# Optimization experiments

Hardware: AMD Instinct MI355X
Metric: run time of the kernel (lower is better)

The kernel has to match this reference:

```python
import jax, jax.numpy as jnp
import numpy as np

N = 100000   # nodes
E = 1600000  # edges
IN = 128
HID = 128
OUT = 64
H = 4
DH = HID // H  # 32
EPS = 1e-5


def gatconv(x, W, al, ar, b, src, dst, heads, dh, act):
    """DGL GATConv: fc -> edge attn (leaky_relu 0.2) -> segment softmax over dst -> scatter sum -> bias -> act."""
    feat = (x @ W).reshape(-1, heads, dh)            # [N,H,dh]
    el = (feat * al).sum(-1)                          # [N,H]
    er = (feat * ar).sum(-1)                          # [N,H]
    e = jax.nn.leaky_relu(el[src] + er[dst], 0.2)     # [E,H]
    m = jax.ops.segment_max(e, dst, num_segments=N)   # [N,H]
    ex = jnp.exp(e - m[dst])                          # [E,H]
    s = jax.ops.segment_sum(ex, dst, num_segments=N)  # [N,H]
    alpha = ex / s[dst]                               # [E,H]
    msg = alpha[:, :, None] * feat[src]               # [E,H,dh]
    out = jax.ops.segment_sum(msg, dst, num_segments=N)  # [N,H,dh]
    out = out + b.reshape(1, heads, dh)
    return act(out) if act is not None else out


def layernorm(x, g, beta):
    mu = x.mean(-1, keepdims=True)
    var = ((x - mu) ** 2).mean(-1, keepdims=True)
    return (x - mu) * jax.lax.rsqrt(var + EPS) * g + beta


def setup_inputs():
    key = jax.random.key(0)
    ks = jax.random.split(key, 24)
    rn = lambda k, shape, s=0.05: jax.random.normal(k, shape, dtype=jnp.float32) * s
    return {
        "x": jax.random.normal(ks[0], (N, IN), dtype=jnp.float32),
        "src": jax.random.randint(ks[1], (E,), 0, N, dtype=jnp.int32),
        "dst": jax.random.randint(ks[2], (E,), 0, N, dtype=jnp.int32),
        "W0": rn(ks[3], (IN, H * DH)), "al0": rn(ks[4], (H, DH)), "ar0": rn(ks[5], (H, DH)), "b0": jnp.zeros((H * DH,), jnp.float32),
        "W1": rn(ks[6], (HID, H * DH)), "al1": rn(ks[7], (H, DH)), "ar1": rn(ks[8], (H, DH)), "b1": jnp.zeros((H * DH,), jnp.float32),
        "W2": rn(ks[9], (HID, HID)), "al2": rn(ks[10], (1, HID)), "ar2": rn(ks[11], (1, HID)), "b2": jnp.zeros((HID,), jnp.float32),
        "g0": jnp.ones((HID,), jnp.float32), "be0": jnp.zeros((HID,), jnp.float32),
        "g1": jnp.ones((HID,), jnp.float32), "be1": jnp.zeros((HID,), jnp.float32),
        "Wc": rn(ks[12], (HID, OUT)), "bc": jnp.zeros((OUT,), jnp.float32),
    }


def reference(x, src, dst, W0, al0, ar0, b0, W1, al1, ar1, b1, W2, al2, ar2, b2,
              g0, be0, g1, be1, Wc, bc):
    # layer 0 (heads=4, elu) -> flatten -> residual -> LN (dropout in eval = identity)
    h_res = x
    h = gatconv(x, W0, al0, ar0, b0, src, dst, H, DH, jax.nn.elu).reshape(N, HID)
    h = layernorm(h + h_res, g0, be0)
    # layer 1 (heads=4, elu)
    h_res = h
    h = gatconv(h, W1, al1, ar1, b1, src, dst, H, DH, jax.nn.elu).reshape(N, HID)
    h = layernorm(h + h_res, g1, be1)
    # layer 2 (heads=1, no activation) -> squeeze -> residual, no norm
    h_res = h
    h = gatconv(h, W2, al2, ar2, b2, src, dst, 1, HID, None).reshape(N, HID)
    h = h + h_res
    embedding = h
    logits = embedding @ Wc + bc
    return (logits, embedding)
```

## Files before the change

### kernel.cpp

```cpp
#include <hip/hip_runtime.h>

#define NN 100000
#define EE 1600000
#define BSHIFT 9
#define NBKT ((NN + 511) / 512)
#define CAP 10240
#define CHUNK 2048
#define NBLKA ((EE + CHUNK - 1) / CHUNK)

typedef float f32x4 __attribute__((ext_vector_type(4)));
typedef float f32x2 __attribute__((ext_vector_type(2)));
typedef short s16x8 __attribute__((ext_vector_type(8)));

__device__ __forceinline__ ushort f2bf(float x) {
  uint u = __float_as_uint(x);
  return (ushort)((u + 0x7fffu + ((u >> 16) & 1u)) >> 16);
}
__device__ __forceinline__ uint pack2bf(float x, float y) {
  return (uint)f2bf(x) | ((uint)f2bf(y) << 16);
}
__device__ __forceinline__ float bflo(uint p) { return __uint_as_float(p << 16); }
__device__ __forceinline__ float bfhi(uint p) { return __uint_as_float(p & 0xffff0000u); }

template<int M, bool ABF, int ELER>
__global__ __launch_bounds__(256) void gemm_mfma(const void* __restrict__ Av,
    const float* __restrict__ W, const float* __restrict__ bias,
    float* __restrict__ outf, ushort* __restrict__ feat8s,
    const float* __restrict__ al, const float* __restrict__ ar,
    float* __restrict__ el, float* __restrict__ er, int N) {
  __shared__ ushort Wt[M * 136];
  const int tid = threadIdx.x;
  for (int idx = tid; idx < 128 * M; idx += 256) {
    int k = idx / M, c = idx - k * M;
    Wt[c * 136 + k] = f2bf(W[idx]);
  }
  __syncthreads();
  const int wid = tid >> 6, lane = tid & 63;
  const int rl = lane & 15, grp = lane >> 4;
  const long row0 = (long)blockIdx.x * 128;

  s16x8 af[2][4];
#pragma unroll
  for (int rt = 0; rt < 2; ++rt) {
    long row = row0 + rt * 64 + wid * 16 + rl;
    if (row >= N) row = N - 1;
    if (ABF) {
      const s16x8* Ar = (const s16x8*)((const ushort*)Av + row * 128);
#pragma unroll
      for (int ks = 0; ks < 4; ++ks) af[rt][ks] = Ar[ks * 4 + grp];
    } else {
      const float4* Ar = (const float4*)((const float*)Av + row * 128);
#pragma unroll
      for (int ks = 0; ks < 4; ++ks) {
        float4 a0 = Ar[ks * 8 + grp * 2];
        float4 a1 = Ar[ks * 8 + grp * 2 + 1];
        s16x8 f;
        f[0] = (short)f2bf(a0.x); f[1] = (short)f2bf(a0.y);
        f[2] = (short)f2bf(a0.z); f[3] = (short)f2bf(a0.w);
        f[4] = (short)f2bf(a1.x); f[5] = (short)f2bf(a1.y);
        f[6] = (short)f2bf(a1.z); f[7] = (short)f2bf(a1.w);
        af[rt][ks] = f;
      }
    }
  }
  const int NT = M / 16;
  f32x4 acc[2][NT];
#pragma unroll
  for (int rt = 0; rt < 2; ++rt)
#pragma unroll
    for (int ct = 0; ct < NT; ++ct) acc[rt][ct] = (f32x4)(0.f);

#pragma unroll
  for (int ct = 0; ct < NT; ++ct) {
#pragma unroll
    for (int ks = 0; ks < 4; ++ks) {
      s16x8 bf = *(const s16x8*)&Wt[(ct * 16 + rl) * 136 + ks * 32 + grp * 8];
      acc[0][ct] = __builtin_amdgcn_mfma_f32_16x16x32_bf16(af[0][ks], bf, acc[0][ct], 0, 0, 0);
      acc[1][ct] = __builtin_amdgcn_mfma_f32_16x16x32_bf16(af[1][ks], bf, acc[1][ct], 0, 0, 0);
    }
  }

  if (ELER > 0) __syncthreads();

#pragma unroll
  for (int rt = 0; rt < 2; ++rt) {
#pragma unroll
    for (int ct = 0; ct < NT; ++ct) {
      int col = ct * 16 + rl;
      float bb = (ELER == 0) ? bias[col] : 0.f;
#pragma unroll
      for (int j = 0; j < 4; ++j) {
        int lrow = rt * 64 + wid * 16 + grp * 4 + j;
        long grow = row0 + lrow;
        if (ELER > 0) {
          Wt[lrow * 128 + col] = f2bf(acc[rt][ct][j]);
        } else if (grow < N) {
          outf[grow * M + col] = acc[rt][ct][j] + bb;
        }
      }
    }
  }

  if (ELER > 0) {
    __syncthreads();
    const uint* stage = (const uint*)Wt;
    float2 a2 = ((const float2*)al)[lane];
    float2 r2 = ((const float2*)ar)[lane];
    for (int rr = 0; rr < 32; ++rr) {
      int lrow = wid * 32 + rr;
      long grow = row0 + lrow;
      uint p = stage[lrow * 64 + lane];
      float x0 = bflo(p), x1 = bfhi(p);
      int pk8 = __builtin_amdgcn_cvt_pk_fp8_f32(x0, x1, 0, false);
      if (grow < N) feat8s[grow * 64 + lane] = (ushort)pk8;
      float pl = x0 * a2.x + x1 * a2.y;
      float pr = x0 * r2.x + x1 * r2.y;
      if (ELER == 4) {
#pragma unroll
        for (int m = 8; m; m >>= 1) {
          pl += __shfl_xor(pl, m, 16);
          pr += __shfl_xor(pr, m, 16);
        }
        if ((lane & 15) == 0 && grow < N) {
          el[grow * 4 + (lane >> 4)] = pl;
          er[grow * 4 + (lane >> 4)] = pr;
        }
      } else {
#pragma unroll
        for (int m = 32; m; m >>= 1) {
          pl += __shfl_xor(pl, m, 64);
          pr += __shfl_xor(pr, m, 64);
        }
        if (lane == 0 && grow < N) { el[grow] = pl; er[grow] = pr; }
      }
    }
  }
}

template<int HEADS>
__global__ __launch_bounds__(256) void wcomp(const int* __restrict__ ssrc,
    const int* __restrict__ sdst, const float* __restrict__ el,
    const float* __restrict__ er, float* __restrict__ wcsr) {
  int e = blockIdx.x * 256 + threadIdx.x;
  if (e >= EE) return;
  int sn = ssrc[e], dn = sdst[e];
  if (HEADS == 4) {
    float4 l4 = ((const float4*)el)[sn];
    float4 r4 = ((const float4*)er)[dn];
    float4 w;
    float ev;
    ev = l4.x + r4.x; ev = fmaxf(ev, 0.f) + 0.2f * fminf(ev, 0.f); w.x = __expf(ev);
    ev = l4.y + r4.y; ev = fmaxf(ev, 0.f) + 0.2f * fminf(ev, 0.f); w.y = __expf(ev);
    ev = l4.z + r4.z; ev = fmaxf(ev, 0.f) + 0.2f * fminf(ev, 0.f); w.z = __expf(ev);
    ev = l4.w + r4.w; ev = fmaxf(ev, 0.f) + 0.2f * fminf(ev, 0.f); w.w = __expf(ev);
    ((float4*)wcsr)[e] = w;
  } else {
    float ev = el[sn] + er[dn];
    ev = fmaxf(ev, 0.f) + 0.2f * fminf(ev, 0.f);
    wcsr[e] = __expf(ev);
  }
}

__global__ __launch_bounds__(256) void k_partA(const int* __restrict__ src,
    const int* __restrict__ dst, uint* __restrict__ bcnt, uint* __restrict__ tmp) {
  __shared__ uint hist[NBKT], excl[NBKT], gbase[NBKT], cur[NBKT];
  __shared__ uint2 recs[CHUNK];
  const int t = threadIdx.x;
  const long e0 = (long)blockIdx.x * CHUNK;
  const int cnt = (EE - e0 < CHUNK) ? (int)(EE - e0) : CHUNK;
  for (int i = t; i < NBKT; i += 256) hist[i] = 0;
  __syncthreads();
  for (int i = t; i < cnt; i += 256) {
    int d = dst[e0 + i];
    atomicAdd(&hist[d >> BSHIFT], 1u);
  }
  __syncthreads();
  if (t == 0) {
    uint run = 0;
    for (int i = 0; i < NBKT; ++i) { excl[i] = run; run += hist[i]; }
  }
  __syncthreads();
  if (t < NBKT) {
    gbase[t] = atomicAdd(&bcnt[t], hist[t]);
    cur[t] = excl[t];
  }
  __syncthreads();
  for (int i = t; i < cnt; i += 256) {
    uint s = (uint)src[e0 + i], d = (uint)dst[e0 + i];
    uint p = atomicAdd(&cur[d >> BSHIFT], 1u);
    recs[p] = make_uint2(s, d);
  }
  __syncthreads();
  for (int i = t; i < cnt; i += 256) {
    uint2 r = recs[i];
    uint b = r.y >> BSHIFT;
    uint pos = gbase[b] + ((uint)i - excl[b]);
    if (pos < CAP) tmp[(long)b * CAP + pos] = r.x | ((r.y & 511u) << 17);
  }
}

__global__ __launch_bounds__(256) void k_bscan(const uint* __restrict__ bcnt,
    uint* __restrict__ bbase, int* __restrict__ indptr) {
  __shared__ uint lds[NBKT];
  int t = threadIdx.x;
  if (t < NBKT) lds[t] = bcnt[t];
  __syncthreads();
  if (t == 0) {
    uint run = 0;
    for (int i = 0; i < NBKT; ++i) { bbase[i] = run; run += lds[i]; }
    indptr[NN] = (int)run;
  }
}

__global__ __launch_bounds__(256) void k_partB(const uint* __restrict__ bcnt,
    const uint* __restrict__ bbase, const uint* __restrict__ tmp,
    int* __restrict__ indptr, int* __restrict__ ssrc, int* __restrict__ sdst) {
  __shared__ uint hist[512], cur[512], wsum[256];
  __shared__ uint stage[CAP];
  const int b = blockIdx.x, t = threadIdx.x;
  const int dlo = b << BSHIFT;
  const int nn = (NN - dlo < 512) ? (NN - dlo) : 512;
  int nrec = (int)bcnt[b];
  if (nrec > CAP) nrec = CAP;
  const uint base = bbase[b];
  const uint* tb = tmp + (long)b * CAP;
  for (int i = t; i < 512; i += 256) hist[i] = 0;
  __syncthreads();
  for (int i = t; i < nrec; i += 256) {
    atomicAdd(&hist[tb[i] >> 17], 1u);
  }
  __syncthreads();
  uint a0 = hist[t * 2], a1 = hist[t * 2 + 1];
  uint ts = a0 + a1;
  wsum[t] = ts;
  __syncthreads();
  for (int st = 1; st < 256; st <<= 1) {
    uint v = (t >= st) ? wsum[t - st] : 0;
    __syncthreads();
    wsum[t] += v;
    __syncthreads();
  }
  uint texcl = wsum[t] - ts;
  cur[t * 2] = texcl;
  cur[t * 2 + 1] = texcl + a0;
  if (t * 2 < nn)     indptr[dlo + t * 2]     = (int)(base + texcl);
  if (t * 2 + 1 < nn) indptr[dlo + t * 2 + 1] = (int)(base + texcl + a0);
  __syncthreads();
  for (int i = t; i < nrec; i += 256) {
    uint v = tb[i];
    uint rel = atomicAdd(&cur[v >> 17], 1u);
    stage[rel] = v;
  }
  __syncthreads();
  for (int i = t; i < nrec; i += 256) {
    uint v = stage[i];
    ssrc[base + i] = (int)(v & 0x1FFFFu);
    sdst[base + i] = dlo + (int)(v >> 17);
  }
}

template<int HEADS, bool FINAL, bool PREVBF>
__global__ __launch_bounds__(256) void gat_aggregate(
    const int* __restrict__ indptr, const int* __restrict__ ssrc,
    const float* __restrict__ wcsr, const char* __restrict__ feat8,
    const float* __restrict__ bias, const void* __restrict__ prevv,
    const float* __restrict__ g, const float* __restrict__ beta,
    void* __restrict__ outv, int N) {
  int wave = threadIdx.x >> 6, lane = threadIdx.x & 63;
  long n = (long)blockIdx.x * 4 + wave;
  if (n >= N) return;
  const int b = __builtin_amdgcn_readfirstlane(indptr[n]);
  const int e = __builtin_amdgcn_readfirstlane(indptr[n + 1]);
  const int deg = e - b;
  const int l5 = lane & 31, half = lane >> 5;
  const int* sp = ssrc + b;
  const float* wlp;
  if (HEADS == 4) wlp = wcsr + (size_t)b * 4 + half * 4 + (l5 >> 3);
  else            wlp = wcsr + (size_t)b + half;
  const uint lpart = (uint)l5 * 4u;

  float a0 = 0.f, a1 = 0.f, a2 = 0.f, a3 = 0.f, s = 0.f;
  const int npair = (deg + 1) >> 1;
  for (int p = 0; p < npair; p += 4) {
#pragma unroll
    for (int k = 0; k < 4; ++k) {
      const int pk = p + k;
      int ja = 2 * pk;     if (ja > deg - 1) ja = deg - 1;
      int jb = 2 * pk + 1; if (jb > deg - 1) jb = deg - 1;
      uint sao = ((uint)sp[ja] & 131071u) << 7;
      uint sbo = ((uint)sp[jb] & 131071u) << 7;
      uint voff = (half ? sbo : sao) + lpart;
      uint v = *(const uint*)(feat8 + voff);
      float w = (HEADS == 4) ? wlp[(size_t)k * 8] : wlp[(size_t)k * 2];
      w = (2 * pk + half < deg) ? w : 0.f;
      auto f01 = __builtin_amdgcn_cvt_pk_f32_fp8((int)v, false);
      auto f23 = __builtin_amdgcn_cvt_pk_f32_fp8((int)v, true);
      s += w;
      a0 = fmaf(w, f01[0], a0);
      a1 = fmaf(w, f01[1], a1);
      a2 = fmaf(w, f23[0], a2);
      a3 = fmaf(w, f23[1], a3);
    }
    wlp += (HEADS == 4) ? 32 : 8;
  }
  a0 += __shfl_xor(a0, 32, 64);
  a1 += __shfl_xor(a1, 32, 64);
  a2 += __shfl_xor(a2, 32, 64);
  a3 += __shfl_xor(a3, 32, 64);
  s  += __shfl_xor(s, 32, 64);

  float inv = (s > 0.f) ? 1.f / s : 0.f;
  float v0 = a0 * inv, v1 = a1 * inv, v2 = a2 * inv, v3 = a3 * inv;
  float4 bb = ((const float4*)bias)[l5];
  v0 += bb.x; v1 += bb.y; v2 += bb.z; v3 += bb.w;
  if (!FINAL) {
    v0 = v0 > 0.f ? v0 : __expf(v0) - 1.f;
    v1 = v1 > 0.f ? v1 : __expf(v1) - 1.f;
    v2 = v2 > 0.f ? v2 : __expf(v2) - 1.f;
    v3 = v3 > 0.f ? v3 : __expf(v3) - 1.f;
  }
  if (PREVBF) {
    uint2 pp = ((const uint2*)prevv)[n * 32 + l5];
    v0 += bflo(pp.x); v1 += bfhi(pp.x);
    v2 += bflo(pp.y); v3 += bfhi(pp.y);
  } else {
    float4 ph = ((const float4*)prevv)[n * 32 + l5];
    v0 += ph.x; v1 += ph.y; v2 += ph.z; v3 += ph.w;
  }
  if (!FINAL) {
    float sum = v0 + v1 + v2 + v3;
#pragma unroll
    for (int m = 16; m; m >>= 1) sum += __shfl_xor(sum, m, 64);
    float mu = sum * (1.f / 128.f);
    float d0 = v0 - mu, d1 = v1 - mu, d2 = v2 - mu, d3 = v3 - mu;
    float vs = d0 * d0 + d1 * d1 + d2 * d2 + d3 * d3;
#pragma unroll
    for (int m = 16; m; m >>= 1) vs += __shfl_xor(vs, m, 64);
    float rstd = rsqrtf(vs * (1.f / 128.f) + 1e-5f);
    float4 g4 = ((const float4*)g)[l5];
    float4 be4 = ((const float4*)beta)[l5];
    float o0 = d0 * rstd * g4.x + be4.x;
    float o1 = d1 * rstd * g4.y + be4.y;
    float o2 = d2 * rstd * g4.z + be4.z;
    float o3 = d3 * rstd * g4.w + be4.w;
    if (!half) ((uint2*)outv)[n * 32 + l5] = make_uint2(pack2bf(o0, o1), pack2bf(o2, o3));
  } else {
    if (!half) ((float4*)outv)[n * 32 + l5] = make_float4(v0, v1, v2, v3);
  }
}

extern "C" void kernel_launch(void* const* d_in, const int* in_sizes, int n_in,
                              void* d_out, int out_size, void* d_ws, size_t ws_size,
                              hipStream_t stream) {
  const float* x   = (const float*)d_in[0];
  const int*   src = (const int*)d_in[1];
  const int*   dst = (const int*)d_in[2];
  const float* W0  = (const float*)d_in[3];
  const float* al0 = (const float*)d_in[4];
  const float* ar0 = (const float*)d_in[5];
  const float* b0  = (const float*)d_in[6];
  const float* W1  = (const float*)d_in[7];
  const float* al1 = (const float*)d_in[8];
  const float* ar1 = (const float*)d_in[9];
  const float* b1  = (const float*)d_in[10];
  const float* W2  = (const float*)d_in[11];
  const float* al2 = (const float*)d_in[12];
  const float* ar2 = (const float*)d_in[13];
  const float* b2  = (const float*)d_in[14];
  const float* g0  = (const float*)d_in[15];
  const float* be0 = (const float*)d_in[16];
  const float* g1  = (const float*)d_in[17];
  const float* be1 = (const float*)d_in[18];
  const float* Wc  = (const float*)d_in[19];
  const float* bc  = (const float*)d_in[20];

  float* out    = (float*)d_out;
  float* logits = out;
  float* emb    = out + (long)NN * 64;

  char*   feat8 = (char*)d_ws;
  float*  el    = (float*)(feat8 + (size_t)NN * 128);
  float*  er    = el + (long)NN * 4;
  ushort* bufAb = (ushort*)(er + (long)NN * 4);
  ushort* bufBb = bufAb + (long)NN * 128;
  float*  wcsrb = (float*)(bufBb + (long)NN * 128);
  int*    sdst  = (int*)(wcsrb + (long)EE * 4);
  uint*   tmp   = (uint*)(sdst + EE);
  uint*   bcnt  = tmp + (long)NBKT * CAP;
  uint*   bbase = bcnt + NBKT;
  ushort* feat8s = (ushort*)feat8;

  int* indptr = (int*)d_out;
  int* ssrc   = indptr + NN + 1;

  const int gN4 = (NN + 3) / 4;
  const int gGm = (NN + 127) / 128;
  const int gE  = (EE + 255) / 256;

  hipMemsetAsync(bcnt, 0, NBKT * sizeof(uint), stream);
  k_partA<<<NBLKA, 256, 0, stream>>>(src, dst, bcnt, tmp);
  k_bscan<<<1, 256, 0, stream>>>(bcnt, bbase, indptr);
  k_partB<<<NBKT, 256, 0, stream>>>(bcnt, bbase, tmp, indptr, ssrc, sdst);

  gemm_mfma<128, false, 4><<<gGm, 256, 0, stream>>>(x, W0, nullptr, nullptr, feat8s, al0, ar0, el, er, NN);
  wcomp<4><<<gE, 256, 0, stream>>>(ssrc, sdst, el, er, wcsrb);
  gat_aggregate<4, false, false><<<gN4, 256, 0, stream>>>(indptr, ssrc, wcsrb, feat8, b0, x, g0, be0, bufAb, NN);

  gemm_mfma<128, true, 4><<<gGm, 256, 0, stream>>>(bufAb, W1, nullptr, nullptr, feat8s, al1, ar1, el, er, NN);
  wcomp<4><<<gE, 256, 0, stream>>>(ssrc, sdst, el, er, wcsrb);
  gat_aggregate<4, false, true><<<gN4, 256, 0, stream>>>(indptr, ssrc, wcsrb, feat8, b1, bufAb, g1, be1, bufBb, NN);

  gemm_mfma<128, true, 1><<<gGm, 256, 0, stream>>>(bufBb, W2, nullptr, nullptr, feat8s, al2, ar2, el, er, NN);
  wcomp<1><<<gE, 256, 0, stream>>>(ssrc, sdst, el, er, wcsrb);
  gat_aggregate<1, true, true><<<gN4, 256, 0, stream>>>(indptr, ssrc, wcsrb, feat8, b2, bufBb, nullptr, nullptr, emb, NN);

  gemm_mfma<64, false, 0><<<gGm, 256, 0, stream>>>(emb, Wc, bc, logits, nullptr, nullptr, nullptr, nullptr, nullptr, NN);
}
```

Before: 362.9 us.

## Process four edges per wave iteration with 8-byte fp8 gathers per lane

Restructures the per-node aggregation so each wave splits into four 16-lane groups, each handling one edge per iteration and loading 8 fp8 features per lane. The old layout used two 32-lane halves with 4 bytes per lane. Accumulation now uses packed f32x2 multiply-adds, and the ragged tail gets a single masked step. The goal is more gather parallelism and wider loads per instruction, at the cost of a two-stage cross-group shuffle reduction and more registers per lane. The old mask of source indices (&131071) is dropped.

```diff
diff --git a/kernel.cpp b/kernel.cpp
--- a/kernel.cpp
+++ b/kernel.cpp
@@ -272,80 +272,116 @@
   const int b = __builtin_amdgcn_readfirstlane(indptr[n]);
   const int e = __builtin_amdgcn_readfirstlane(indptr[n + 1]);
   const int deg = e - b;
-  const int l5 = lane & 31, half = lane >> 5;
+  const int l4 = lane & 15, q = lane >> 4;
+  const int head = (HEADS == 4) ? (l4 >> 2) : 0;
   const int* sp = ssrc + b;
-  const float* wlp;
-  if (HEADS == 4) wlp = wcsr + (size_t)b * 4 + half * 4 + (l5 >> 3);
-  else            wlp = wcsr + (size_t)b + half;
-  const uint lpart = (uint)l5 * 4u;
-
-  float a0 = 0.f, a1 = 0.f, a2 = 0.f, a3 = 0.f, s = 0.f;
-  const int npair = (deg + 1) >> 1;
-  for (int p = 0; p < npair; p += 4) {
-#pragma unroll
-    for (int k = 0; k < 4; ++k) {
-      const int pk = p + k;
-      int ja = 2 * pk;     if (ja > deg - 1) ja = deg - 1;
-      int jb = 2 * pk + 1; if (jb > deg - 1) jb = deg - 1;
-      uint sao = ((uint)sp[ja] & 131071u) << 7;
-      uint sbo = ((uint)sp[jb] & 131071u) << 7;
-      uint voff = (half ? sbo : sao) + lpart;
-      uint v = *(const uint*)(feat8 + voff);
-      float w = (HEADS == 4) ? wlp[(size_t)k * 8] : wlp[(size_t)k * 2];
-      w = (2 * pk + half < deg) ? w : 0.f;
-      auto f01 = __builtin_amdgcn_cvt_pk_f32_fp8((int)v, false);
-      auto f23 = __builtin_amdgcn_cvt_pk_f32_fp8((int)v, true);
-      s += w;
-      a0 = fmaf(w, f01[0], a0);
-      a1 = fmaf(w, f01[1], a1);
-      a2 = fmaf(w, f23[0], a2);
-      a3 = fmaf(w, f23[1], a3);
-    }
-    wlp += (HEADS == 4) ? 32 : 8;
-  }
-  a0 += __shfl_xor(a0, 32, 64);
-  a1 += __shfl_xor(a1, 32, 64);
-  a2 += __shfl_xor(a2, 32, 64);
-  a3 += __shfl_xor(a3, 32, 64);
-  s  += __shfl_xor(s, 32, 64);
+  const float* wl = wcsr + (size_t)b * HEADS + q * HEADS + head;
+  const uint lpart = (uint)l4 * 8u;
+
+  f32x2 ac0 = {0.f, 0.f}, ac1 = {0.f, 0.f}, ac2 = {0.f, 0.f}, ac3 = {0.f, 0.f};
+  float s = 0.f;
+  const int ngrp = deg >> 2;
+#pragma unroll 2
+  for (int kk = 0; kk < ngrp; ++kk) {
+    int sn0 = sp[4 * kk + 0], sn1 = sp[4 * kk + 1];
+    int sn2 = sp[4 * kk + 2], sn3 = sp[4 * kk + 3];
+    uint so0 = (uint)sn0 << 7, so1 = (uint)sn1 << 7;
+    uint so2 = (uint)sn2 << 7, so3 = (uint)sn3 << 7;
+    uint so = (q == 0) ? so0 : (q == 1) ? so1 : (q == 2) ? so2 : so3;
+    uint2 v = *(const uint2*)(feat8 + (so + lpart));
+    float w = wl[(size_t)kk * 4 * HEADS];
+    s += w;
+    f32x2 w2 = {w, w};
+    ac0 += w2 * __builtin_amdgcn_cvt_pk_f32_fp8((int)v.x, false);
+    ac1 += w2 * __builtin_amdgcn_cvt_pk_f32_fp8((int)v.x, true);
+    ac2 += w2 * __builtin_amdgcn_cvt_pk_f32_fp8((int)v.y, false);
+    ac3 += w2 * __builtin_amdgcn_cvt_pk_f32_fp8((int)v.y, true);
+  }
+  if (deg & 3) {
+    int j = 4 * ngrp + q;
+    int jc = j < deg - 1 ? j : deg - 1;
+    uint sn = (uint)ssrc[b + jc];
+    uint2 v = *(const uint2*)(feat8 + (((uint)sn << 7) + lpart));
+    float w = wcsr[(size_t)(b + jc) * HEADS + head];
+    w = (j < deg) ? w : 0.f;
+    s += w;
+    f32x2 w2 = {w, w};
+    ac0 += w2 * __builtin_amdgcn_cvt_pk_f32_fp8((int)v.x, false);
+    ac1 += w2 * __builtin_amdgcn_cvt_pk_f32_fp8((int)v.x, true);
+    ac2 += w2 * __builtin_amdgcn_cvt_pk_f32_fp8((int)v.y, false);
+    ac3 += w2 * __builtin_amdgcn_cvt_pk_f32_fp8((int)v.y, true);
+  }
+#pragma unroll
+  for (int m = 16; m <= 32; m <<= 1) {
+    ac0[0] += __shfl_xor(ac0[0], m, 64); ac0[1] += __shfl_xor(ac0[1], m, 64);
+    ac1[0] += __shfl_xor(ac1[0], m, 64); ac1[1] += __shfl_xor(ac1[1], m, 64);
+    ac2[0] += __shfl_xor(ac2[0], m, 64); ac2[1] += __shfl_xor(ac2[1], m, 64);
+    ac3[0] += __shfl_xor(ac3[0], m, 64); ac3[1] += __shfl_xor(ac3[1], m, 64);
+    s += __shfl_xor(s, m, 64);
+  }
 
   float inv = (s > 0.f) ? 1.f / s : 0.f;
-  float v0 = a0 * inv, v1 = a1 * inv, v2 = a2 * inv, v3 = a3 * inv;
-  float4 bb = ((const float4*)bias)[l5];
-  v0 += bb.x; v1 += bb.y; v2 += bb.z; v3 += bb.w;
+  float v0 = ac0[0] * inv, v1 = ac0[1] * inv, v2 = ac1[0] * inv, v3 = ac1[1] * inv;
+  float v4 = ac2[0] * inv, v5 = ac2[1] * inv, v6 = ac3[0] * inv, v7 = ac3[1] * inv;
+  float4 bl = ((const float4*)bias)[l4 * 2];
+  float4 bh = ((const float4*)bias)[l4 * 2 + 1];
+  v0 += bl.x; v1 += bl.y; v2 += bl.z; v3 += bl.w;
+  v4 += bh.x; v5 += bh.y; v6 += bh.z; v7 += bh.w;
   if (!FINAL) {
     v0 = v0 > 0.f ? v0 : __expf(v0) - 1.f;
     v1 = v1 > 0.f ? v1 : __expf(v1) - 1.f;
     v2 = v2 > 0.f ? v2 : __expf(v2) - 1.f;
     v3 = v3 > 0.f ? v3 : __expf(v3) - 1.f;
+    v4 = v4 > 0.f ? v4 : __expf(v4) - 1.f;
+    v5 = v5 > 0.f ? v5 : __expf(v5) - 1.f;
+    v6 = v6 > 0.f ? v6 : __expf(v6) - 1.f;
+    v7 = v7 > 0.f ? v7 : __expf(v7) - 1.f;
   }
   if (PREVBF) {
-    uint2 pp = ((const uint2*)prevv)[n * 32 + l5];
+    uint4 pp = ((const uint4*)prevv)[n * 16 + l4];
     v0 += bflo(pp.x); v1 += bfhi(pp.x);
     v2 += bflo(pp.y); v3 += bfhi(pp.y);
+    v4 += bflo(pp.z); v5 += bfhi(pp.z);
+    v6 += bflo(pp.w); v7 += bfhi(pp.w);
   } else {
-    float4 ph = ((const float4*)prevv)[n * 32 + l5];
-    v0 += ph.x; v1 += ph.y; v2 += ph.z; v3 += ph.w;
+    float4 pl = ((const float4*)prevv)[n * 32 + l4 * 2];
+    float4 ph = ((const float4*)prevv)[n * 32 + l4 * 2 + 1];
+    v0 += pl.x; v1 += pl.y; v2 += pl.z; v3 += pl.w;
+    v4 += ph.x; v5 += ph.y; v6 += ph.z; v7 += ph.w;
   }
   if (!FINAL) {
-    float sum = v0 + v1 + v2 + v3;
-#pragma unroll
-    for (int m = 16; m; m >>= 1) sum += __shfl_xor(sum, m, 64);
+    float sum = ((v0 + v1) + (v2 + v3)) + ((v4 + v5) + (v6 + v7));
+#pragma unroll
+    for (int m = 8; m; m >>= 1) sum += __shfl_xor(sum, m, 64);
     float mu = sum * (1.f / 128.f);
     float d0 = v0 - mu, d1 = v1 - mu, d2 = v2 - mu, d3 = v3 - mu;
-    float vs = d0 * d0 + d1 * d1 + d2 * d2 + d3 * d3;
-#pragma unroll
-    for (int m = 16; m; m >>= 1) vs += __shfl_xor(vs, m, 64);
+    float d4 = v4 - mu, d5 = v5 - mu, d6 = v6 - mu, d7 = v7 - mu;
+    float vs = ((d0 * d0 + d1 * d1) + (d2 * d2 + d3 * d3)) +
+               ((d4 * d4 + d5 * d5) + (d6 * d6 + d7 * d7));
+#pragma unroll
+    for (int m = 8; m; m >>= 1) vs += __shfl_xor(vs, m, 64);
     float rstd = rsqrtf(vs * (1.f / 128.f) + 1e-5f);
-    float4 g4 = ((const float4*)g)[l5];
-    float4 be4 = ((const float4*)beta)[l5];
-    float o0 = d0 * rstd * g4.x + be4.x;
-    float o1 = d1 * rstd * g4.y + be4.y;
-    float o2 = d2 * rstd * g4.z + be4.z;
-    float o3 = d3 * rstd * g4.w + be4.w;
-    if (!half) ((uint2*)outv)[n * 32 + l5] = make_uint2(pack2bf(o0, o1), pack2bf(o2, o3));
+    float4 g4l = ((const float4*)g)[l4 * 2];
+    float4 g4h = ((const float4*)g)[l4 * 2 + 1];
+    float4 bel = ((const float4*)beta)[l4 * 2];
+    float4 beh = ((const float4*)beta)[l4 * 2 + 1];
+    float o0 = d0 * rstd * g4l.x + bel.x;
+    float o1 = d1 * rstd * g4l.y + bel.y;
+    float o2 = d2 * rstd * g4l.z + bel.z;
+    float o3 = d3 * rstd * g4l.w + bel.w;
+    float o4 = d4 * rstd * g4h.x + beh.x;
+    float o5 = d5 * rstd * g4h.y + beh.y;
+    float o6 = d6 * rstd * g4h.z + beh.z;
+    float o7 = d7 * rstd * g4h.w + beh.w;
+    if (q == 0) {
+      uint4 ov;
+      ov.x = pack2bf(o0, o1); ov.y = pack2bf(o2, o3);
+      ov.z = pack2bf(o4, o5); ov.w = pack2bf(o6, o7);
+      ((uint4*)outv)[n * 16 + l4] = ov;
+    }
   } else {
-    if (!half) ((float4*)outv)[n * 32 + l5] = make_float4(v0, v1, v2, v3);
+    if (q == 0) ((float4*)outv)[n * 32 + l4 * 2] = make_float4(v0, v1, v2, v3);
+    if (q == 1) ((float4*)outv)[n * 32 + l4 * 2 + 1] = make_float4(v4, v5, v6, v7);
   }
 }
 
```

After: 389.5 us. +7.3%, slower.

## Fuse edge attention weights into aggregation and feed bf16 embedding to classifier

Applied to the files above, without the earlier changes.

Removes the separate per-edge weight kernel and its sdst array. The aggregation kernel now gathers el of each source node, adds the destination's er, and applies leaky_relu and exp inline. This avoids writing and re-reading a 1.6M x 4 float weight buffer three times and drops three launches, at the cost of redundant exp work across lanes. The final layer also writes a bf16 copy of the embedding, so the classifier GEMM reads bf16 input instead of fp32, which slightly lowers logits precision.

```diff
diff --git a/kernel.cpp b/kernel.cpp
--- a/kernel.cpp
+++ b/kernel.cpp
@@ -137,30 +137,6 @@
   }
 }
 
-template<int HEADS>
-__global__ __launch_bounds__(256) void wcomp(const int* __restrict__ ssrc,
-    const int* __restrict__ sdst, const float* __restrict__ el,
-    const float* __restrict__ er, float* __restrict__ wcsr) {
-  int e = blockIdx.x * 256 + threadIdx.x;
-  if (e >= EE) return;
-  int sn = ssrc[e], dn = sdst[e];
-  if (HEADS == 4) {
-    float4 l4 = ((const float4*)el)[sn];
-    float4 r4 = ((const float4*)er)[dn];
-    float4 w;
-    float ev;
-    ev = l4.x + r4.x; ev = fmaxf(ev, 0.f) + 0.2f * fminf(ev, 0.f); w.x = __expf(ev);
-    ev = l4.y + r4.y; ev = fmaxf(ev, 0.f) + 0.2f * fminf(ev, 0.f); w.y = __expf(ev);
-    ev = l4.z + r4.z; ev = fmaxf(ev, 0.f) + 0.2f * fminf(ev, 0.f); w.z = __expf(ev);
-    ev = l4.w + r4.w; ev = fmaxf(ev, 0.f) + 0.2f * fminf(ev, 0.f); w.w = __expf(ev);
-    ((float4*)wcsr)[e] = w;
-  } else {
-    float ev = el[sn] + er[dn];
-    ev = fmaxf(ev, 0.f) + 0.2f * fminf(ev, 0.f);
-    wcsr[e] = __expf(ev);
-  }
-}
-
 __global__ __launch_bounds__(256) void k_partA(const int* __restrict__ src,
     const int* __restrict__ dst, uint* __restrict__ bcnt, uint* __restrict__ tmp) {
   __shared__ uint hist[NBKT], excl[NBKT], gbase[NBKT], cur[NBKT];
@@ -214,7 +190,7 @@
 
 __global__ __launch_bounds__(256) void k_partB(const uint* __restrict__ bcnt,
     const uint* __restrict__ bbase, const uint* __restrict__ tmp,
-    int* __restrict__ indptr, int* __restrict__ ssrc, int* __restrict__ sdst) {
+    int* __restrict__ indptr, int* __restrict__ ssrc) {
   __shared__ uint hist[512], cur[512], wsum[256];
   __shared__ uint stage[CAP];
   const int b = blockIdx.x, t = threadIdx.x;
@@ -253,19 +229,18 @@
   }
   __syncthreads();
   for (int i = t; i < nrec; i += 256) {
-    uint v = stage[i];
-    ssrc[base + i] = (int)(v & 0x1FFFFu);
-    sdst[base + i] = dlo + (int)(v >> 17);
+    ssrc[base + i] = (int)(stage[i] & 0x1FFFFu);
   }
 }
 
 template<int HEADS, bool FINAL, bool PREVBF>
 __global__ __launch_bounds__(256) void gat_aggregate(
     const int* __restrict__ indptr, const int* __restrict__ ssrc,
-    const float* __restrict__ wcsr, const char* __restrict__ feat8,
-    const float* __restrict__ bias, const void* __restrict__ prevv,
-    const float* __restrict__ g, const float* __restrict__ beta,
-    void* __restrict__ outv, int N) {
+    const char* __restrict__ el8, const float* __restrict__ er,
+    const char* __restrict__ feat8, const float* __restrict__ bias,
+    const void* __restrict__ prevv, const float* __restrict__ g,
+    const float* __restrict__ beta, void* __restrict__ outv,
+    ushort* __restrict__ embb, int N) {
   int wave = threadIdx.x >> 6, lane = threadIdx.x & 63;
   long n = (long)blockIdx.x * 4 + wave;
   if (n >= N) return;
@@ -273,11 +248,11 @@
   const int e = __builtin_amdgcn_readfirstlane(indptr[n + 1]);
   const int deg = e - b;
   const int l5 = lane & 31, half = lane >> 5;
+  const int head = (HEADS == 4) ? (l5 >> 3) : 0;
+  const float er0 = (HEADS == 4) ? er[n * 4 + head] : er[n];
   const int* sp = ssrc + b;
-  const float* wlp;
-  if (HEADS == 4) wlp = wcsr + (size_t)b * 4 + half * 4 + (l5 >> 3);
-  else            wlp = wcsr + (size_t)b + half;
   const uint lpart = (uint)l5 * 4u;
+  const uint hoff = (uint)head * 4u;
 
   float a0 = 0.f, a1 = 0.f, a2 = 0.f, a3 = 0.f, s = 0.f;
   const int npair = (deg + 1) >> 1;
@@ -287,11 +262,15 @@
       const int pk = p + k;
       int ja = 2 * pk;     if (ja > deg - 1) ja = deg - 1;
       int jb = 2 * pk + 1; if (jb > deg - 1) jb = deg - 1;
-      uint sao = ((uint)sp[ja] & 131071u) << 7;
-      uint sbo = ((uint)sp[jb] & 131071u) << 7;
-      uint voff = (half ? sbo : sao) + lpart;
-      uint v = *(const uint*)(feat8 + voff);
-      float w = (HEADS == 4) ? wlp[(size_t)k * 8] : wlp[(size_t)k * 2];
+      uint sna = (uint)sp[ja], snb = (uint)sp[jb];
+      uint fo = ((half ? snb : sna) << 7) + lpart;
+      uint v = *(const uint*)(feat8 + fo);
+      float elv;
+      if (HEADS == 4) elv = *(const float*)(el8 + (((half ? snb : sna) << 4) + hoff));
+      else            elv = *(const float*)(el8 + ((half ? snb : sna) << 2));
+      float ev = elv + er0;
+      ev = fmaxf(ev, 0.f) + 0.2f * fminf(ev, 0.f);
+      float w = __expf(ev);
       w = (2 * pk + half < deg) ? w : 0.f;
       auto f01 = __builtin_amdgcn_cvt_pk_f32_fp8((int)v, false);
       auto f23 = __builtin_amdgcn_cvt_pk_f32_fp8((int)v, true);
@@ -301,7 +280,6 @@
       a2 = fmaf(w, f23[0], a2);
       a3 = fmaf(w, f23[1], a3);
     }
-    wlp += (HEADS == 4) ? 32 : 8;
   }
   a0 += __shfl_xor(a0, 32, 64);
   a1 += __shfl_xor(a1, 32, 64);
@@ -345,7 +323,10 @@
     float o3 = d3 * rstd * g4.w + be4.w;
     if (!half) ((uint2*)outv)[n * 32 + l5] = make_uint2(pack2bf(o0, o1), pack2bf(o2, o3));
   } else {
-    if (!half) ((float4*)outv)[n * 32 + l5] = make_float4(v0, v1, v2, v3);
+    if (!half) {
+      ((float4*)outv)[n * 32 + l5] = make_float4(v0, v1, v2, v3);
+      ((uint2*)embb)[n * 32 + l5] = make_uint2(pack2bf(v0, v1), pack2bf(v2, v3));
+    }
   }
 }
 
@@ -383,36 +364,31 @@
   float*  er    = el + (long)NN * 4;
   ushort* bufAb = (ushort*)(er + (long)NN * 4);
   ushort* bufBb = bufAb + (long)NN * 128;
-  float*  wcsrb = (float*)(bufBb + (long)NN * 128);
-  int*    sdst  = (int*)(wcsrb + (long)EE * 4);
-  uint*   tmp   = (uint*)(sdst + EE);
+  uint*   tmp   = (uint*)(bufBb + (long)NN * 128);
   uint*   bcnt  = tmp + (long)NBKT * CAP;
   uint*   bbase = bcnt + NBKT;
   ushort* feat8s = (ushort*)feat8;
+  char*   el8   = (char*)el;
 
   int* indptr = (int*)d_out;
   int* ssrc   = indptr + NN + 1;
 
   const int gN4 = (NN + 3) / 4;
   const int gGm = (NN + 127) / 128;
-  const int gE  = (EE + 255) / 256;
 
   hipMemsetAsync(bcnt, 0, NBKT * sizeof(uint), stream);
   k_partA<<<NBLKA, 256, 0, stream>>>(src, dst, bcnt, tmp);
   k_bscan<<<1, 256, 0, stream>>>(bcnt, bbase, indptr);
-  k_partB<<<NBKT, 256, 0, stream>>>(bcnt, bbase, tmp, indptr, ssrc, sdst);
+  k_partB<<<NBKT, 256, 0, stream>>>(bcnt, bbase, tmp, indptr, ssrc);
 
   gemm_mfma<128, false, 4><<<gGm, 256, 0, stream>>>(x, W0, nullptr, nullptr, feat8s, al0, ar0, el, er, NN);
-  wcomp<4><<<gE, 256, 0, stream>>>(ssrc, sdst, el, er, wcsrb);
-  gat_aggregate<4, false, false><<<gN4, 256, 0, stream>>>(indptr, ssrc, wcsrb, feat8, b0, x, g0, be0, bufAb, NN);
+  gat_aggregate<4, false, false><<<gN4, 256, 0, stream>>>(indptr, ssrc, el8, er, feat8, b0, x, g0, be0, bufAb, nullptr, NN);
 
   gemm_mfma<128, true, 4><<<gGm, 256, 0, stream>>>(bufAb, W1, nullptr, nullptr, feat8s, al1, ar1, el, er, NN);
-  wcomp<4><<<gE, 256, 0, stream>>>(ssrc, sdst, el, er, wcsrb);
-  gat_aggregate<4, false, true><<<gN4, 256, 0, stream>>>(indptr, ssrc, wcsrb, feat8, b1, bufAb, g1, be1, bufBb, NN);
+  gat_aggregate<4, false, true><<<gN4, 256, 0, stream>>>(indptr, ssrc, el8, er, feat8, b1, bufAb, g1, be1, bufBb, nullptr, NN);
 
   gemm_mfma<128, true, 1><<<gGm, 256, 0, stream>>>(bufBb, W2, nullptr, nullptr, feat8s, al2, ar2, el, er, NN);
-  wcomp<1><<<gE, 256, 0, stream>>>(ssrc, sdst, el, er, wcsrb);
-  gat_aggregate<1, true, true><<<gN4, 256, 0, stream>>>(indptr, ssrc, wcsrb, feat8, b2, bufBb, nullptr, nullptr, emb, NN);
-
-  gemm_mfma<64, false, 0><<<gGm, 256, 0, stream>>>(emb, Wc, bc, logits, nullptr, nullptr, nullptr, nullptr, nullptr, NN);
-}
+  gat_aggregate<1, true, true><<<gN4, 256, 0, stream>>>(indptr, ssrc, el8, er, feat8, b2, bufBb, nullptr, nullptr, emb, bufAb, NN);
+
+  gemm_mfma<64, true, 0><<<gGm, 256, 0, stream>>>(bufAb, Wc, bc, logits, nullptr, nullptr, nullptr, nullptr, nullptr, NN);
+}
```

Result: faster. 337.1 us (-7.1%).
